# Kernel tuning notes

Hardware: AMD Instinct MI355X
Metric: run time of the kernel (lower is better)

## Reference

```python
import jax, jax.numpy as jnp
import numpy as np

K = 2            # top-k experts per sample
LOSS_COEF = 0.01


def _cv_squared(v):
    eps = 1e-10
    return jnp.var(v, ddof=1) / (jnp.mean(v) ** 2 + eps)


def setup_inputs() -> dict:
    key = jax.random.key(0)
    k1, k2, k3, k4 = jax.random.split(key, 4)
    B, S, D, O, E = 32, 512, 768, 768, 8
    return {
        "x": jax.random.normal(k1, (B, S, D), dtype=jnp.float32),
        "w_gate": jax.random.normal(k2, (D, E), dtype=jnp.float32) * 0.02,
        "weight": jax.random.normal(k3, (E, O, D), dtype=jnp.float32) * 0.02,
        "bias": jax.random.normal(k4, (E, O), dtype=jnp.float32) * 0.02,
    }


def reference(x, w_gate, weight, bias):
    # x: [B, S, D]; w_gate: [D, E]; weight: [E, O, D]; bias: [E, O]
    B = x.shape[0]
    E = w_gate.shape[1]

    # --- top-k gating (eval mode: clean logits, no noise) ---
    pooled = x.mean(-2)                       # [B, D] (moe_level != 'task'/'token')
    logits = pooled @ w_gate                  # [B, E]
    top_vals, top_idx = jax.lax.top_k(logits, min(K + 1, E))
    tk_vals, tk_idx = top_vals[:, :K], top_idx[:, :K]
    tk_gates = jax.nn.softmax(tk_vals, axis=1)            # [B, K]
    gates = jnp.zeros_like(logits).at[jnp.arange(B)[:, None], tk_idx].set(tk_gates)  # [B, E]

    load = (gates > 0).sum(0).astype(jnp.float32)          # [E]
    importance = gates.sum(0)                              # [E]
    loss = (_cv_squared(importance) + _cv_squared(load)) * LOSS_COEF

    # --- per-sample soft combination of expert weights, then batched linear ---
    # same math as sum_e gates[b,e] * weight[e] without materializing [B,E,O,D]
    expert_w = jnp.einsum('be,eoi->boi', gates, weight)    # [B, O, D]
    expert_b = jnp.einsum('be,eo->bo', gates, bias)        # [B, O]
    y = jnp.einsum('bij,bkj->bik', x, expert_w) + expert_b[:, None, :]  # [B, S, O]
    return (y, loss)
```

## Files before the change

kernel.cpp:

```cpp
#include <hip/hip_runtime.h>
#include <hip/hip_bf16.h>
#include <stdint.h>

#define B_ 32
#define S_ 512
#define D_ 768
#define O_ 768
#define E_ 8
#define YSIZE (B_ * S_ * O_)
#define BK 32
#define NSTEP (D_ / BK)
#define WSLICE (O_ * D_)

typedef __attribute__((ext_vector_type(8))) short bf16x8;
typedef __attribute__((ext_vector_type(4))) float f32x4;

static __device__ __forceinline__ unsigned short f2bf(float f) {
  union { float f; uint32_t u; } v; v.f = f;
  uint32_t u = v.u;
  uint32_t r = u + 0x7fff + ((u >> 16) & 1);
  return (unsigned short)(r >> 16);
}

static __device__ __forceinline__ void async_load16(const void* g, void* l) {
  __builtin_amdgcn_global_load_lds(
      (const __attribute__((address_space(1))) void*)g,
      (__attribute__((address_space(3))) void*)l, 16, 0, 0);
}

__global__ __launch_bounds__(192) void k_pool_convert(
    const float* __restrict__ x, unsigned short* __restrict__ xb,
    float* __restrict__ psum) {
  int t  = threadIdx.x;
  int b  = blockIdx.x;
  int sc = blockIdx.y;
  size_t rowbase = (size_t)(b * S_ + sc * 32) * D_;
  const float* xp = x + rowbase + 4 * t;
  unsigned short* op = xb + rowbase + 4 * t;
  float4 sum = {0.f, 0.f, 0.f, 0.f};
  #pragma unroll 8
  for (int s = 0; s < 32; ++s) {
    float4 v = *(const float4*)(xp + (size_t)s * D_);
    sum.x += v.x; sum.y += v.y; sum.z += v.z; sum.w += v.w;
    ushort4 o;
    o.x = f2bf(v.x); o.y = f2bf(v.y); o.z = f2bf(v.z); o.w = f2bf(v.w);
    *(ushort4*)(op + (size_t)s * D_) = o;
  }
  *(float4*)(psum + (size_t)(b * 16 + sc) * D_ + 4 * t) = sum;
}

__global__ __launch_bounds__(256) void k_logits(
    const float* __restrict__ psum, const float* __restrict__ w_gate,
    float* __restrict__ gates, int* __restrict__ eidx,
    float* __restrict__ gval) {
  int b = blockIdx.x;
  int tid = threadIdx.x;
  float acc[E_];
  #pragma unroll
  for (int e = 0; e < E_; ++e) acc[e] = 0.f;

  for (int d = tid; d < D_; d += 256) {
    float p = 0.f;
    #pragma unroll
    for (int c = 0; c < 16; ++c) p += psum[(size_t)(b * 16 + c) * D_ + d];
    p *= (1.0f / (float)S_);
    const float* wg = w_gate + d * E_;
    #pragma unroll
    for (int e = 0; e < E_; ++e) acc[e] += p * wg[e];
  }
  #pragma unroll
  for (int off = 32; off > 0; off >>= 1) {
    #pragma unroll
    for (int e = 0; e < E_; ++e) acc[e] += __shfl_down(acc[e], off, 64);
  }
  __shared__ float part[4][E_];
  if ((tid & 63) == 0) {
    #pragma unroll
    for (int e = 0; e < E_; ++e) part[tid >> 6][e] = acc[e];
  }
  __syncthreads();
  if (tid == 0) {
    float lg[E_];
    #pragma unroll
    for (int e = 0; e < E_; ++e)
      lg[e] = part[0][e] + part[1][e] + part[2][e] + part[3][e];
    int i0 = 0; float v0 = lg[0];
    #pragma unroll
    for (int e = 1; e < E_; ++e) { if (lg[e] > v0) { v0 = lg[e]; i0 = e; } }
    int i1 = -1; float v1 = -1e30f;
    #pragma unroll
    for (int e = 0; e < E_; ++e) {
      if (e == i0) continue;
      if (lg[e] > v1) { v1 = lg[e]; i1 = e; }
    }
    float m  = fmaxf(v0, v1);
    float x0 = expf(v0 - m), x1 = expf(v1 - m);
    float s  = x0 + x1;
    float g0 = x0 / s, g1 = x1 / s;
    #pragma unroll
    for (int e = 0; e < E_; ++e)
      gates[b * E_ + e] = (e == i0) ? g0 : ((e == i1) ? g1 : 0.f);
    eidx[b] = i0; eidx[B_ + b] = i1;
    gval[b] = g0; gval[B_ + b] = g1;
  }
}

__global__ __launch_bounds__(256) void k_combine(
    const float* __restrict__ weight, const float* __restrict__ gates,
    unsigned short* __restrict__ wc, float* __restrict__ loss_out) {
  __shared__ float gsh[B_][E_];
  int tid = threadIdx.x;
  if (tid < B_ * E_) ((float*)gsh)[tid] = gates[tid];
  __syncthreads();

  if (blockIdx.x == 0 && tid == 0) {
    double mi = 0, ml = 0;
    float imp[E_], ldv[E_];
    #pragma unroll
    for (int e = 0; e < E_; ++e) {
      float s = 0.f, c = 0.f;
      for (int b = 0; b < B_; ++b) {
        float g = gsh[b][e];
        s += g; c += (g > 0.f) ? 1.f : 0.f;
      }
      imp[e] = s; ldv[e] = c;
      mi += s; ml += c;
    }
    mi /= E_; ml /= E_;
    double vi = 0, vl = 0;
    #pragma unroll
    for (int e = 0; e < E_; ++e) {
      double di = imp[e] - mi, dl = ldv[e] - ml;
      vi += di * di; vl += dl * dl;
    }
    vi /= (E_ - 1); vl /= (E_ - 1);
    loss_out[0] = (float)((vi / (mi * mi + 1e-10) + vl / (ml * ml + 1e-10)) * 0.01);
  }

  size_t i = (size_t)blockIdx.x * 1024 + (size_t)tid * 4;
  float v[E_][4];
  #pragma unroll
  for (int e = 0; e < E_; ++e) {
    float4 u = *(const float4*)(weight + (size_t)e * WSLICE + i);
    v[e][0] = u.x; v[e][1] = u.y; v[e][2] = u.z; v[e][3] = u.w;
  }
  #pragma unroll 4
  for (int b = 0; b < B_; ++b) {
    float c[4];
    #pragma unroll
    for (int j = 0; j < 4; ++j) c[j] = 0.f;
    #pragma unroll
    for (int e = 0; e < E_; ++e) {
      float g = gsh[b][e];
      #pragma unroll
      for (int j = 0; j < 4; ++j) c[j] += g * v[e][j];
    }
    uint32_t p0 = (uint32_t)f2bf(c[0]) | ((uint32_t)f2bf(c[1]) << 16);
    uint32_t p1 = (uint32_t)f2bf(c[2]) | ((uint32_t)f2bf(c[3]) << 16);
    *(uint2*)(wc + (size_t)b * WSLICE + i) = make_uint2(p0, p1);
  }
}

__global__ __launch_bounds__(256, 3) void k_moe_gemm(
    const unsigned short* __restrict__ xb, const unsigned short* __restrict__ wc,
    const int* __restrict__ eidx, const float* __restrict__ gval,
    const float* __restrict__ bias, float* __restrict__ y) {
  __shared__ unsigned short Alds[2][128 * BK];
  __shared__ unsigned short Blds[2][128 * BK];

  int flat = blockIdx.x;
  int xcd  = flat & 7;
  int slot = flat >> 3;
  int b    = xcd + 8 * (slot / 24);
  int tile = slot % 24;
  int st = tile & 3;
  int ot = tile >> 2;
  int s0 = st * 128, o0 = ot * 128;

  int tid  = threadIdx.x;
  int wave = tid >> 6, lane = tid & 63;
  int wm = wave & 1, wn = wave >> 1;

  const unsigned short* Abase = xb + ((size_t)(b * S_ + s0)) * D_;
  const unsigned short* Bbase = wc + (size_t)b * WSLICE + (size_t)o0 * D_;

  f32x4 acc[4][4];
  #pragma unroll
  for (int i = 0; i < 4; ++i)
    #pragma unroll
    for (int j = 0; j < 4; ++j) acc[i][j] = (f32x4){0.f, 0.f, 0.f, 0.f};

  int a_chunk0 = wave * 2;
  int a_r = lane >> 2;
  int a_c = (((lane & 3) ^ ((a_r >> 1) & 3))) * 8;

  int sseg  = lane >> 4;
  int r16   = lane & 15;
  int kphys = (sseg ^ ((r16 >> 1) & 3)) * 8;

  auto stage = [&](int buf, int kk) {
    #pragma unroll
    for (int j = 0; j < 2; ++j) {
      int chunk = a_chunk0 + j;
      const unsigned short* srcA =
          Abase + (size_t)(chunk * 16 + a_r) * D_ + kk + a_c;
      async_load16(srcA, &Alds[buf][chunk * 512]);
      const unsigned short* srcB =
          Bbase + (size_t)(chunk * 16 + a_r) * D_ + kk + a_c;
      async_load16(srcB, &Blds[buf][chunk * 512]);
    }
  };

  auto compute = [&](int buf) {
    bf16x8 af[4], bfr[4];
    #pragma unroll
    for (int mi = 0; mi < 4; ++mi)
      af[mi] = *(const bf16x8*)(&Alds[buf][(wm * 64 + mi * 16 + r16) * BK + kphys]);
    #pragma unroll
    for (int ni = 0; ni < 4; ++ni)
      bfr[ni] = *(const bf16x8*)(&Blds[buf][(wn * 64 + ni * 16 + r16) * BK + kphys]);
    #pragma unroll
    for (int mi = 0; mi < 4; ++mi)
      #pragma unroll
      for (int ni = 0; ni < 4; ++ni)
        acc[mi][ni] = __builtin_amdgcn_mfma_f32_16x16x32_bf16(
            af[mi], bfr[ni], acc[mi][ni], 0, 0, 0);
  };

  stage(0, 0);
  __syncthreads();

  #pragma unroll 1
  for (int tt = 0; tt < 11; ++tt) {
    stage(1, (2 * tt + 1) * BK);
    compute(0);
    __syncthreads();
    stage(0, (2 * tt + 2) * BK);
    compute(1);
    __syncthreads();
  }
  stage(1, 23 * BK);
  compute(0);
  __syncthreads();
  compute(1);

  int   e0 = eidx[b], e1 = eidx[B_ + b];
  float g0 = gval[b], g1 = gval[B_ + b];
  float* Y = y + ((size_t)(b * S_ + s0)) * O_ + o0;
  int col   = lane & 15;
  int rquad = (lane >> 4) * 4;
  #pragma unroll
  for (int ni = 0; ni < 4; ++ni) {
    int n = wn * 64 + ni * 16 + col;
    float cbv = g0 * bias[e0 * O_ + o0 + n] + g1 * bias[e1 * O_ + o0 + n];
    #pragma unroll
    for (int mi = 0; mi < 4; ++mi) {
      #pragma unroll
      for (int r = 0; r < 4; ++r) {
        int m = wm * 64 + mi * 16 + rquad + r;
        Y[(size_t)m * O_ + n] = acc[mi][ni][r] + cbv;
      }
    }
  }
}

extern "C" void kernel_launch(void* const* d_in, const int* in_sizes, int n_in,
                              void* d_out, int out_size, void* d_ws, size_t ws_size,
                              hipStream_t stream) {
  const float* x      = (const float*)d_in[0];
  const float* w_gate = (const float*)d_in[1];
  const float* weight = (const float*)d_in[2];
  const float* bias   = (const float*)d_in[3];
  float* y = (float*)d_out;

  float* psum  = (float*)d_ws;
  float* gates = (float*)((char*)d_ws + 1572864);
  int*   eidx  = (int*)((char*)d_ws + 1573888);
  float* gval  = (float*)((char*)d_ws + 1574144);
  unsigned short* xb = (unsigned short*)((char*)d_ws + 2097152);
  unsigned short* wc = (unsigned short*)((char*)d_ws + 27262976);

  k_pool_convert<<<dim3(32, 16), 192, 0, stream>>>(x, xb, psum);
  k_logits<<<32, 256, 0, stream>>>(psum, w_gate, gates, eidx, gval);
  k_combine<<<576, 256, 0, stream>>>(weight, gates, wc, y + YSIZE);
  k_moe_gemm<<<768, 256, 0, stream>>>(xb, wc, eidx, gval, bias, y);
}
```

Baseline: 161.4 us.

## Fuse expert weight combination into GEMM B-tile staging, drop combine kernel

Removes the separate k_combine kernel that materialized a per-sample bf16 combined weight tensor. The GEMM now loads the two selected experts' fp32 weight rows directly, blends them with the gate values in registers, converts with v_cvt_pk_bf16_f32 and writes the result to LDS. The loss is computed in the GEMM's first block, and the barriers are replaced with explicit waitcnt plus s_barrier. This saves one launch and the write and re-read of the combined weights, but each tile now does synchronous fp32 global loads of two experts and extra ALU work, and the same blends are recomputed across tiles that share weights.

```diff
diff --git a/kernel.cpp b/kernel.cpp
--- a/kernel.cpp
+++ b/kernel.cpp
@@ -9,7 +9,6 @@
 #define E_ 8
 #define YSIZE (B_ * S_ * O_)
 #define BK 32
-#define NSTEP (D_ / BK)
 #define WSLICE (O_ * D_)
 
 typedef __attribute__((ext_vector_type(8))) short bf16x8;
@@ -20,6 +19,12 @@
   uint32_t u = v.u;
   uint32_t r = u + 0x7fff + ((u >> 16) & 1);
   return (unsigned short)(r >> 16);
+}
+
+static __device__ __forceinline__ uint32_t cvt_pk_bf16(float lo, float hi) {
+  uint32_t r;
+  asm("v_cvt_pk_bf16_f32 %0, %1, %2" : "=v"(r) : "v"(lo), "v"(hi));
+  return r;
 }
 
 static __device__ __forceinline__ void async_load16(const void* g, void* l) {
@@ -51,8 +56,7 @@
 
 __global__ __launch_bounds__(256) void k_logits(
     const float* __restrict__ psum, const float* __restrict__ w_gate,
-    float* __restrict__ gates, int* __restrict__ eidx,
-    float* __restrict__ gval) {
+    int* __restrict__ eidx, float* __restrict__ gval) {
   int b = blockIdx.x;
   int tid = threadIdx.x;
   float acc[E_];
@@ -96,75 +100,16 @@
     float m  = fmaxf(v0, v1);
     float x0 = expf(v0 - m), x1 = expf(v1 - m);
     float s  = x0 + x1;
-    float g0 = x0 / s, g1 = x1 / s;
-    #pragma unroll
-    for (int e = 0; e < E_; ++e)
-      gates[b * E_ + e] = (e == i0) ? g0 : ((e == i1) ? g1 : 0.f);
     eidx[b] = i0; eidx[B_ + b] = i1;
-    gval[b] = g0; gval[B_ + b] = g1;
-  }
-}
-
-__global__ __launch_bounds__(256) void k_combine(
-    const float* __restrict__ weight, const float* __restrict__ gates,
-    unsigned short* __restrict__ wc, float* __restrict__ loss_out) {
-  __shared__ float gsh[B_][E_];
-  int tid = threadIdx.x;
-  if (tid < B_ * E_) ((float*)gsh)[tid] = gates[tid];
-  __syncthreads();
-
-  if (blockIdx.x == 0 && tid == 0) {
-    double mi = 0, ml = 0;
-    float imp[E_], ldv[E_];
-    #pragma unroll
-    for (int e = 0; e < E_; ++e) {
-      float s = 0.f, c = 0.f;
-      for (int b = 0; b < B_; ++b) {
-        float g = gsh[b][e];
-        s += g; c += (g > 0.f) ? 1.f : 0.f;
-      }
-      imp[e] = s; ldv[e] = c;
-      mi += s; ml += c;
-    }
-    mi /= E_; ml /= E_;
-    double vi = 0, vl = 0;
-    #pragma unroll
-    for (int e = 0; e < E_; ++e) {
-      double di = imp[e] - mi, dl = ldv[e] - ml;
-      vi += di * di; vl += dl * dl;
-    }
-    vi /= (E_ - 1); vl /= (E_ - 1);
-    loss_out[0] = (float)((vi / (mi * mi + 1e-10) + vl / (ml * ml + 1e-10)) * 0.01);
-  }
-
-  size_t i = (size_t)blockIdx.x * 1024 + (size_t)tid * 4;
-  float v[E_][4];
-  #pragma unroll
-  for (int e = 0; e < E_; ++e) {
-    float4 u = *(const float4*)(weight + (size_t)e * WSLICE + i);
-    v[e][0] = u.x; v[e][1] = u.y; v[e][2] = u.z; v[e][3] = u.w;
-  }
-  #pragma unroll 4
-  for (int b = 0; b < B_; ++b) {
-    float c[4];
-    #pragma unroll
-    for (int j = 0; j < 4; ++j) c[j] = 0.f;
-    #pragma unroll
-    for (int e = 0; e < E_; ++e) {
-      float g = gsh[b][e];
-      #pragma unroll
-      for (int j = 0; j < 4; ++j) c[j] += g * v[e][j];
-    }
-    uint32_t p0 = (uint32_t)f2bf(c[0]) | ((uint32_t)f2bf(c[1]) << 16);
-    uint32_t p1 = (uint32_t)f2bf(c[2]) | ((uint32_t)f2bf(c[3]) << 16);
-    *(uint2*)(wc + (size_t)b * WSLICE + i) = make_uint2(p0, p1);
+    gval[b] = x0 / s; gval[B_ + b] = x1 / s;
   }
 }
 
 __global__ __launch_bounds__(256, 3) void k_moe_gemm(
-    const unsigned short* __restrict__ xb, const unsigned short* __restrict__ wc,
+    const unsigned short* __restrict__ xb, const float* __restrict__ weight,
     const int* __restrict__ eidx, const float* __restrict__ gval,
-    const float* __restrict__ bias, float* __restrict__ y) {
+    const float* __restrict__ bias, float* __restrict__ y,
+    float* __restrict__ loss_out) {
   __shared__ unsigned short Alds[2][128 * BK];
   __shared__ unsigned short Blds[2][128 * BK];
 
@@ -182,7 +127,43 @@
   int wm = wave & 1, wn = wave >> 1;
 
   const unsigned short* Abase = xb + ((size_t)(b * S_ + s0)) * D_;
-  const unsigned short* Bbase = wc + (size_t)b * WSLICE + (size_t)o0 * D_;
+
+  if (flat == 0 && tid == 0) {
+    float imp[E_], ldv[E_];
+    #pragma unroll
+    for (int e = 0; e < E_; ++e) { imp[e] = 0.f; ldv[e] = 0.f; }
+    for (int bb = 0; bb < 2 * B_; ++bb) {
+      imp[eidx[bb]] += gval[bb];
+      ldv[eidx[bb]] += 1.f;
+    }
+    double mi = 0, ml = 0;
+    #pragma unroll
+    for (int e = 0; e < E_; ++e) { mi += imp[e]; ml += ldv[e]; }
+    mi /= E_; ml /= E_;
+    double vi = 0, vl = 0;
+    #pragma unroll
+    for (int e = 0; e < E_; ++e) {
+      double di = imp[e] - mi, dl = ldv[e] - ml;
+      vi += di * di; vl += dl * dl;
+    }
+    vi /= (E_ - 1); vl /= (E_ - 1);
+    loss_out[0] = (float)((vi / (mi * mi + 1e-10) + vl / (ml * ml + 1e-10)) * 0.01);
+  }
+
+  int   e0 = eidx[b], e1 = eidx[B_ + b];
+  float g0 = gval[b], g1 = gval[B_ + b];
+  int col   = lane & 15;
+  int rquad = (lane >> 4) * 4;
+  float cbv[4];
+  #pragma unroll
+  for (int ni = 0; ni < 4; ++ni) {
+    int n = wn * 64 + ni * 16 + col;
+    cbv[ni] = g0 * bias[e0 * O_ + o0 + n] + g1 * bias[e1 * O_ + o0 + n];
+  }
+  asm volatile("s_waitcnt vmcnt(0)" ::: "memory");
+
+  const float* W0 = weight + (size_t)e0 * WSLICE;
+  const float* W1 = weight + (size_t)e1 * WSLICE;
 
   f32x4 acc[4][4];
   #pragma unroll
@@ -199,15 +180,37 @@
   int kphys = (sseg ^ ((r16 >> 1) & 3)) * 8;
 
   auto stage = [&](int buf, int kk) {
+    float4 w[8];
+    #pragma unroll
+    for (int j = 0; j < 2; ++j) {
+      int row = o0 + (a_chunk0 + j) * 16 + a_r;
+      const float* p0 = W0 + (size_t)row * D_ + kk + a_c;
+      const float* p1 = W1 + (size_t)row * D_ + kk + a_c;
+      w[j * 4 + 0] = *(const float4*)(p0);
+      w[j * 4 + 1] = *(const float4*)(p0 + 4);
+      w[j * 4 + 2] = *(const float4*)(p1);
+      w[j * 4 + 3] = *(const float4*)(p1 + 4);
+    }
     #pragma unroll
     for (int j = 0; j < 2; ++j) {
       int chunk = a_chunk0 + j;
       const unsigned short* srcA =
           Abase + (size_t)(chunk * 16 + a_r) * D_ + kk + a_c;
       async_load16(srcA, &Alds[buf][chunk * 512]);
-      const unsigned short* srcB =
-          Bbase + (size_t)(chunk * 16 + a_r) * D_ + kk + a_c;
-      async_load16(srcB, &Blds[buf][chunk * 512]);
+    }
+    asm volatile("s_waitcnt vmcnt(2)" ::: "memory");
+    #pragma unroll
+    for (int j = 0; j < 2; ++j) {
+      int chunk = a_chunk0 + j;
+      float4 a0 = w[j * 4 + 0], a1 = w[j * 4 + 1];
+      float4 b0 = w[j * 4 + 2], b1 = w[j * 4 + 3];
+      uint32_t pk[4];
+      pk[0] = cvt_pk_bf16(g0 * a0.x + g1 * b0.x, g0 * a0.y + g1 * b0.y);
+      pk[1] = cvt_pk_bf16(g0 * a0.z + g1 * b0.z, g0 * a0.w + g1 * b0.w);
+      pk[2] = cvt_pk_bf16(g0 * a1.x + g1 * b1.x, g0 * a1.y + g1 * b1.y);
+      pk[3] = cvt_pk_bf16(g0 * a1.z + g1 * b1.z, g0 * a1.w + g1 * b1.w);
+      *(uint4*)((char*)&Blds[buf][chunk * 512] + lane * 16) =
+          make_uint4(pk[0], pk[1], pk[2], pk[3]);
     }
   };
 
@@ -227,38 +230,44 @@
             af[mi], bfr[ni], acc[mi][ni], 0, 0, 0);
   };
 
+  #define LGKB  do { asm volatile("s_waitcnt lgkmcnt(0)" ::: "memory"); \
+                     __builtin_amdgcn_s_barrier(); } while (0)
+  #define FENB  do { asm volatile("" ::: "memory"); \
+                     __builtin_amdgcn_s_barrier(); } while (0)
+
   stage(0, 0);
-  __syncthreads();
 
   #pragma unroll 1
   for (int tt = 0; tt < 11; ++tt) {
     stage(1, (2 * tt + 1) * BK);
+    LGKB;
     compute(0);
-    __syncthreads();
+    FENB;
     stage(0, (2 * tt + 2) * BK);
+    LGKB;
     compute(1);
-    __syncthreads();
+    FENB;
   }
   stage(1, 23 * BK);
+  LGKB;
   compute(0);
-  __syncthreads();
+  asm volatile("s_waitcnt vmcnt(0)" ::: "memory");
+  __builtin_amdgcn_s_barrier();
   compute(1);
 
-  int   e0 = eidx[b], e1 = eidx[B_ + b];
-  float g0 = gval[b], g1 = gval[B_ + b];
+  #undef LGKB
+  #undef FENB
+
   float* Y = y + ((size_t)(b * S_ + s0)) * O_ + o0;
-  int col   = lane & 15;
-  int rquad = (lane >> 4) * 4;
   #pragma unroll
   for (int ni = 0; ni < 4; ++ni) {
     int n = wn * 64 + ni * 16 + col;
-    float cbv = g0 * bias[e0 * O_ + o0 + n] + g1 * bias[e1 * O_ + o0 + n];
     #pragma unroll
     for (int mi = 0; mi < 4; ++mi) {
       #pragma unroll
       for (int r = 0; r < 4; ++r) {
         int m = wm * 64 + mi * 16 + rquad + r;
-        Y[(size_t)m * O_ + n] = acc[mi][ni][r] + cbv;
+        Y[(size_t)m * O_ + n] = acc[mi][ni][r] + cbv[ni];
       }
     }
   }
@@ -274,14 +283,12 @@
   float* y = (float*)d_out;
 
   float* psum  = (float*)d_ws;
-  float* gates = (float*)((char*)d_ws + 1572864);
   int*   eidx  = (int*)((char*)d_ws + 1573888);
   float* gval  = (float*)((char*)d_ws + 1574144);
   unsigned short* xb = (unsigned short*)((char*)d_ws + 2097152);
-  unsigned short* wc = (unsigned short*)((char*)d_ws + 27262976);
 
   k_pool_convert<<<dim3(32, 16), 192, 0, stream>>>(x, xb, psum);
-  k_logits<<<32, 256, 0, stream>>>(psum, w_gate, gates, eidx, gval);
-  k_combine<<<576, 256, 0, stream>>>(weight, gates, wc, y + YSIZE);
-  k_moe_gemm<<<768, 256, 0, stream>>>(xb, wc, eidx, gval, bias, y);
-}
+  k_logits<<<32, 256, 0, stream>>>(psum, w_gate, eidx, gval);
+  k_moe_gemm<<<768, 256, 0, stream>>>(xb, weight, eidx, gval, bias, y,
+                                      y + YSIZE);
+}
```

Measured after the change: 174.6 us. 1.08x slower.
